# Kernel optimization log

Measured on AMD Instinct MI355X. Metric: run time of the kernel, lower is better.

The kernel has to match this reference:

```python
import jax, jax.numpy as jnp
import numpy as np

B, T, H = 64, 1024, 1024


def setup_inputs() -> dict:
    key = jax.random.key(0)
    ks = jax.random.split(key, 8)
    s = 1.0 / np.sqrt(H)
    return {
        "spatial_feats": jax.random.normal(ks[0], (B, T, H), dtype=jnp.float32),
        "hidden_state": jax.random.normal(ks[1], (B, H), dtype=jnp.float32),
        "W_enc": jax.random.uniform(ks[2], (H, H), jnp.float32, -s, s),
        "b_enc": jax.random.uniform(ks[3], (H,), jnp.float32, -s, s),
        "W_dec": jax.random.uniform(ks[4], (H, H), jnp.float32, -s, s),
        "b_dec": jax.random.uniform(ks[5], (H,), jnp.float32, -s, s),
        "w_score": jax.random.uniform(ks[6], (H,), jnp.float32, -s, s),
        "b_score": jax.random.uniform(ks[7], (), jnp.float32, -s, s),
    }


def reference(spatial_feats, hidden_state, W_enc, b_enc, W_dec, b_dec, w_score, b_score):
    # decoder_proj(hidden_state): [B, H] -> [B, 1, H]
    dec = (jnp.einsum("bh,oh->bo", hidden_state, W_dec) + b_dec)[:, None, :]
    # encoder_proj(spatial_feats): [B, T, H]
    enc = jnp.einsum("bth,oh->bto", spatial_feats, W_enc) + b_enc
    energy = jnp.tanh(enc + dec)                      # [B, T, H]
    scores = jnp.einsum("bth,h->bt", energy, w_score) + b_score  # [B, T]
    weights = jax.nn.softmax(scores, axis=1)          # [B, T]
    context = jnp.einsum("bth,bt->bh", spatial_feats, weights)   # [B, H]
    return (context, weights)
```

## Files before the change

kernel.cpp:

```cpp
#include <hip/hip_runtime.h>
#include <hip/hip_bf16.h>
#include <math.h>


typedef __attribute__((ext_vector_type(8))) short bf16x8;
typedef __attribute__((ext_vector_type(8))) unsigned short ushort8;
typedef __attribute__((ext_vector_type(4))) float f32x4;

__device__ __forceinline__ unsigned short f2bf(float f) {
  union { float f; unsigned int u; } v; v.f = f;
  unsigned int r = v.u + 0x7FFFu + ((v.u >> 16) & 1u);
  return (unsigned short)(r >> 16);
}

__device__ __forceinline__ float bf2f(unsigned short b) {
  union { unsigned int u; float f; } v; v.u = ((unsigned int)b) << 16;
  return v.f;
}

__device__ __forceinline__ float fast_tanh(float x) {
  float e = __expf(2.0f * x);
  return 1.0f - 2.0f / (e + 1.0f);
}

__device__ __forceinline__ void gld16(const void* g, void* l) {
  __builtin_amdgcn_global_load_lds(
      (const __attribute__((address_space(1))) void*)g,
      (__attribute__((address_space(3))) void*)l, 16, 0, 0);
}

__global__ __launch_bounds__(256) void prep_kernel(
    const float* __restrict__ spatial, const float* __restrict__ hidden,
    const float* __restrict__ W_enc, const float* __restrict__ b_enc,
    const float* __restrict__ W_dec, const float* __restrict__ b_dec,
    unsigned short* __restrict__ Wbf, unsigned short* __restrict__ Abf,
    float* __restrict__ dec, int nW, int nA) {
  __shared__ float hs[1024];
  const int bid = blockIdx.x, tid = threadIdx.x;
  if (bid < nW + nA) {
    const float* src = (bid < nW) ? W_enc : spatial;
    unsigned short* dst = (bid < nW) ? Wbf : Abf;
    size_t g4 = (size_t)(bid < nW ? bid : bid - nW) * 256 + tid;
    float4 v = ((const float4*)src)[g4];
    ushort4 o;
    o.x = f2bf(v.x); o.y = f2bf(v.y); o.z = f2bf(v.z); o.w = f2bf(v.w);
    *(ushort4*)(dst + g4 * 4) = o;
    return;
  }
  const int dbid = bid - nW - nA;
  const int b = dbid >> 3, o0 = (dbid & 7) * 128;
  const int wave = tid >> 6, lane = tid & 63;
  ((float4*)hs)[tid] = ((const float4*)(hidden + (size_t)b * 1024))[tid];
  __syncthreads();
  for (int it = 0; it < 32; it++) {
    int o = o0 + it * 4 + wave;
    const float4* w4 = (const float4*)(W_dec + (size_t)o * 1024);
    float4 acc; acc.x = acc.y = acc.z = acc.w = 0.f;
    #pragma unroll
    for (int j = 0; j < 4; j++) {
      int i = j * 64 + lane;
      float4 x = ((const float4*)hs)[i], y = w4[i];
      acc.x = fmaf(x.x, y.x, acc.x);
      acc.y = fmaf(x.y, y.y, acc.y);
      acc.z = fmaf(x.z, y.z, acc.z);
      acc.w = fmaf(x.w, y.w, acc.w);
    }
    float v = (acc.x + acc.y) + (acc.z + acc.w);
    #pragma unroll
    for (int off = 1; off < 64; off <<= 1) v += __shfl_xor(v, off);
    if (lane == 0) dec[b * 1024 + o] = v + b_dec[o] + b_enc[o];
  }
}

__global__ __launch_bounds__(256) void enc_score_bf16_kernel(
    const unsigned short* __restrict__ A,
    const unsigned short* __restrict__ W,
    const float* __restrict__ dec,
    const float* __restrict__ w_score,
    float* __restrict__ scores_p)
{
  __shared__ unsigned short As[2][128][32];
  __shared__ unsigned short Bs[2][128][32];

  const int bid = blockIdx.x;
  const int swz = (bid & 7) * 512 + (bid >> 3);
  const int n0 = (swz & 7) * 128;
  const int m0 = (swz >> 3) * 128;
  const int tid = threadIdx.x;
  const int lane = tid & 63, wave = tid >> 6;
  const int wm = (wave >> 1) * 64, wn = (wave & 1) * 64;
  const int quad = lane >> 4, colL = lane & 15;

  const int srow = wave * 32 + (lane >> 2);
  const int scol = (lane & 3) * 8;
  const unsigned short* ga = A + (size_t)(m0 + srow) * 1024 + scol;
  const unsigned short* gb = W + (size_t)(n0 + srow) * 1024 + scol;
  unsigned short* la = &As[0][0][0] + wave * 1024;
  unsigned short* lb = &Bs[0][0][0] + wave * 1024;

  f32x4 acc[4][4];
  #pragma unroll
  for (int mi = 0; mi < 4; mi++)
    #pragma unroll
    for (int ni = 0; ni < 4; ni++)
      acc[mi][ni] = (f32x4){0.f, 0.f, 0.f, 0.f};

  for (int k0 = 0; k0 < 1024; k0 += 64) {
    gld16(ga + k0,                  la);
    gld16(ga + k0 + 16 * 1024,      la + 512);
    gld16(ga + k0 + 32,             la + 4096);
    gld16(ga + k0 + 32 + 16 * 1024, la + 4608);
    gld16(gb + k0,                  lb);
    gld16(gb + k0 + 16 * 1024,      lb + 512);
    gld16(gb + k0 + 32,             lb + 4096);
    gld16(gb + k0 + 32 + 16 * 1024, lb + 4608);
    __syncthreads();
    #pragma unroll
    for (int h = 0; h < 2; h++) {
      bf16x8 af[4], bfr[4];
      #pragma unroll
      for (int i = 0; i < 4; i++) {
        af[i]  = *(const bf16x8*)(&As[h][wm + i * 16 + colL][quad * 8]);
        bfr[i] = *(const bf16x8*)(&Bs[h][wn + i * 16 + colL][quad * 8]);
      }
      #pragma unroll
      for (int mi = 0; mi < 4; mi++)
        #pragma unroll
        for (int ni = 0; ni < 4; ni++)
          acc[mi][ni] = __builtin_amdgcn_mfma_f32_16x16x32_bf16(
              af[mi], bfr[ni], acc[mi][ni], 0, 0, 0);
    }
    __syncthreads();
  }

  const int b = m0 >> 10;
  float decv[4], wsv[4];
  #pragma unroll
  for (int ni = 0; ni < 4; ni++) {
    int n = n0 + wn + ni * 16 + colL;
    decv[ni] = dec[b * 1024 + n];
    wsv[ni] = w_score[n];
  }
  const int slot = (swz & 7) * 2 + (wave & 1);
  #pragma unroll
  for (int mi = 0; mi < 4; mi++) {
    float rs[4] = {0.f, 0.f, 0.f, 0.f};
    #pragma unroll
    for (int ni = 0; ni < 4; ni++)
      #pragma unroll
      for (int r = 0; r < 4; r++)
        rs[r] += fast_tanh(acc[mi][ni][r] + decv[ni]) * wsv[ni];
    #pragma unroll
    for (int r = 0; r < 4; r++) {
      float v = rs[r];
      v += __shfl_xor(v, 1);
      v += __shfl_xor(v, 2);
      v += __shfl_xor(v, 4);
      v += __shfl_xor(v, 8);
      if (colL == 0)
        scores_p[slot * 65536 + m0 + wm + mi * 16 + quad * 4 + r] = v;
    }
  }
}

__global__ __launch_bounds__(256) void enc_score_f32_kernel(
    const float* __restrict__ A, const float* __restrict__ W,
    const float* __restrict__ dec, const float* __restrict__ w_score,
    float* __restrict__ scores_p) {
  __shared__ unsigned short As[128][32];
  __shared__ unsigned short Bs[128][32];
  const int bid = blockIdx.x;
  const int n0 = (bid & 7) * 128;
  const int m0 = (bid >> 3) * 128;
  const int tid = threadIdx.x;
  const int lane = tid & 63, wave = tid >> 6;
  const int wm = (wave >> 1) * 64, wn = (wave & 1) * 64;
  const int quad = lane >> 4, colL = lane & 15;
  const int srow = tid >> 3;
  const int scol = (tid & 7) * 4;
  f32x4 acc[4][4];
  #pragma unroll
  for (int mi = 0; mi < 4; mi++)
    #pragma unroll
    for (int ni = 0; ni < 4; ni++)
      acc[mi][ni] = (f32x4){0.f, 0.f, 0.f, 0.f};
  for (int k0 = 0; k0 < 1024; k0 += 32) {
    #pragma unroll
    for (int p = 0; p < 4; p++) {
      int r = p * 32 + srow;
      float4 va = *(const float4*)(A + (size_t)(m0 + r) * 1024 + (k0 + scol));
      float4 vb = *(const float4*)(W + (size_t)(n0 + r) * 1024 + (k0 + scol));
      ushort4 pa, pb;
      pa.x = f2bf(va.x); pa.y = f2bf(va.y); pa.z = f2bf(va.z); pa.w = f2bf(va.w);
      pb.x = f2bf(vb.x); pb.y = f2bf(vb.y); pb.z = f2bf(vb.z); pb.w = f2bf(vb.w);
      *(ushort4*)(&As[r][scol]) = pa;
      *(ushort4*)(&Bs[r][scol]) = pb;
    }
    __syncthreads();
    bf16x8 af[4], bfr[4];
    #pragma unroll
    for (int i = 0; i < 4; i++) {
      af[i]  = *(const bf16x8*)(&As[wm + i * 16 + colL][quad * 8]);
      bfr[i] = *(const bf16x8*)(&Bs[wn + i * 16 + colL][quad * 8]);
    }
    #pragma unroll
    for (int mi = 0; mi < 4; mi++)
      #pragma unroll
      for (int ni = 0; ni < 4; ni++)
        acc[mi][ni] = __builtin_amdgcn_mfma_f32_16x16x32_bf16(
            af[mi], bfr[ni], acc[mi][ni], 0, 0, 0);
    __syncthreads();
  }
  const int b = m0 >> 10;
  float decv[4], wsv[4];
  #pragma unroll
  for (int ni = 0; ni < 4; ni++) {
    int n = n0 + wn + ni * 16 + colL;
    decv[ni] = dec[b * 1024 + n];
    wsv[ni] = w_score[n];
  }
  const int slot = (bid & 7) * 2 + (wave & 1);
  #pragma unroll
  for (int mi = 0; mi < 4; mi++) {
    float rsv[4] = {0.f, 0.f, 0.f, 0.f};
    #pragma unroll
    for (int ni = 0; ni < 4; ni++)
      #pragma unroll
      for (int r = 0; r < 4; r++)
        rsv[r] += fast_tanh(acc[mi][ni][r] + decv[ni]) * wsv[ni];
    #pragma unroll
    for (int r = 0; r < 4; r++) {
      float v = rsv[r];
      v += __shfl_xor(v, 1);
      v += __shfl_xor(v, 2);
      v += __shfl_xor(v, 4);
      v += __shfl_xor(v, 8);
      if (colL == 0)
        scores_p[slot * 65536 + m0 + wm + mi * 16 + quad * 4 + r] = v;
    }
  }
}

__global__ void softmax_kernel(const float* __restrict__ scores_p,
                               float* __restrict__ weights,
                               float* __restrict__ context) {
  __shared__ float red[256];
  int b = blockIdx.x, tid = threadIdx.x;
  float4 z; z.x = z.y = z.z = z.w = 0.f;
  ((float4*)context)[blockIdx.x * 256 + tid] = z;
  float v[4];
  float mx = -1e30f;
  #pragma unroll
  for (int i = 0; i < 4; i++) {
    int m = b * 1024 + tid + i * 256;
    float s = 0.f;
    #pragma unroll
    for (int sl = 0; sl < 16; sl++) s += scores_p[sl * 65536 + m];
    v[i] = s;
    mx = fmaxf(mx, v[i]);
  }
  red[tid] = mx; __syncthreads();
  for (int off = 128; off > 0; off >>= 1) {
    if (tid < off) red[tid] = fmaxf(red[tid], red[tid + off]);
    __syncthreads();
  }
  mx = red[0]; __syncthreads();
  float sum = 0.f;
  #pragma unroll
  for (int i = 0; i < 4; i++) { v[i] = __expf(v[i] - mx); sum += v[i]; }
  red[tid] = sum; __syncthreads();
  for (int off = 128; off > 0; off >>= 1) {
    if (tid < off) red[tid] += red[tid + off];
    __syncthreads();
  }
  float inv = 1.0f / red[0];
  #pragma unroll
  for (int i = 0; i < 4; i++) weights[b * 1024 + tid + i * 256] = v[i] * inv;
}

__global__ void context_bf16_kernel(const unsigned short* __restrict__ Abf,
                                    const float* __restrict__ weights,
                                    float* __restrict__ context) {
  int b = blockIdx.x >> 3, tq = blockIdx.x & 7;
  int tid = threadIdx.x;
  __shared__ float wl[128];
  __shared__ float cs[128 * 8];
  if (tid < 128) wl[tid] = weights[b * 1024 + tq * 128 + tid];
  __syncthreads();
  const int hl = tid & 127, p = tid >> 7;
  const int h0 = hl * 8;
  const unsigned short* sp =
      Abf + ((size_t)(b * 1024 + tq * 128 + p)) * 1024 + h0;
  float acc[8];
  #pragma unroll
  for (int j = 0; j < 8; j++) acc[j] = 0.f;
  for (int t = 0; t < 128; t += 2) {
    float w = wl[t + p];
    ushort8 x = *(const ushort8*)(sp + (size_t)t * 1024);
    #pragma unroll
    for (int j = 0; j < 8; j++) acc[j] = fmaf(w, bf2f(x[j]), acc[j]);
  }
  if (p == 0) {
    #pragma unroll
    for (int j = 0; j < 8; j++) cs[hl * 8 + j] = acc[j];
  }
  __syncthreads();
  if (p == 1) {
    #pragma unroll
    for (int j = 0; j < 8; j++) cs[hl * 8 + j] += acc[j];
  }
  __syncthreads();
  if (p == 0) {
    #pragma unroll
    for (int j = 0; j < 8; j++)
      atomicAdd(&context[b * 1024 + h0 + j], cs[hl * 8 + j]);
  }
}

__global__ void context_f32_kernel(const float* __restrict__ spatial,
                                   const float* __restrict__ weights,
                                   float* __restrict__ context) {
  int b = blockIdx.x >> 3, tq = blockIdx.x & 7;
  int tid = threadIdx.x;
  __shared__ float wl[128];
  if (tid < 128) wl[tid] = weights[b * 1024 + tq * 128 + tid];
  __syncthreads();
  const float4* sp =
      (const float4*)(spatial + ((size_t)(b * 1024 + tq * 128)) * 1024);
  float4 acc; acc.x = acc.y = acc.z = acc.w = 0.f;
  #pragma unroll 4
  for (int t = 0; t < 128; t++) {
    float w = wl[t];
    float4 x = sp[(size_t)t * 256 + tid];
    acc.x = fmaf(w, x.x, acc.x);
    acc.y = fmaf(w, x.y, acc.y);
    acc.z = fmaf(w, x.z, acc.z);
    acc.w = fmaf(w, x.w, acc.w);
  }
  float* c = context + b * 1024 + tid * 4;
  atomicAdd(c + 0, acc.x);
  atomicAdd(c + 1, acc.y);
  atomicAdd(c + 2, acc.z);
  atomicAdd(c + 3, acc.w);
}

extern "C" void kernel_launch(void* const* d_in, const int* in_sizes, int n_in,
                              void* d_out, int out_size, void* d_ws, size_t ws_size,
                              hipStream_t stream) {
  const float* spatial  = (const float*)d_in[0];
  const float* hidden   = (const float*)d_in[1];
  const float* W_enc    = (const float*)d_in[2];
  const float* b_enc    = (const float*)d_in[3];
  const float* W_dec    = (const float*)d_in[4];
  const float* b_dec    = (const float*)d_in[5];
  const float* w_score  = (const float*)d_in[6];

  float* out      = (float*)d_out;
  float* context  = out;
  float* weights  = out + 65536;

  float* scores_p = (float*)d_ws;
  float* dec      = scores_p + 16 * 65536;
  unsigned short* Wbf = (unsigned short*)(dec + 65536);
  unsigned short* Abf = Wbf + 1024 * 1024;

  const size_t need =
      16ull * 65536 * 4 + 65536 * 4 + 2ull * 1024 * 1024 + 2ull * 65536 * 1024;

  if (ws_size >= need) {
    const int nW = 1024, nA = 65536;
    prep_kernel<<<nW + nA + 512, 256, 0, stream>>>(
        spatial, hidden, W_enc, b_enc, W_dec, b_dec, Wbf, Abf, dec, nW, nA);
    enc_score_bf16_kernel<<<4096, 256, 0, stream>>>(Abf, Wbf, dec, w_score,
                                                    scores_p);
    softmax_kernel<<<64, 256, 0, stream>>>(scores_p, weights, context);
    context_bf16_kernel<<<512, 256, 0, stream>>>(Abf, weights, context);
  } else {
    prep_kernel<<<512, 256, 0, stream>>>(
        spatial, hidden, W_enc, b_enc, W_dec, b_dec, nullptr, nullptr, dec,
        0, 0);
    enc_score_f32_kernel<<<4096, 256, 0, stream>>>(spatial, W_enc, dec,
                                                   w_score, scores_p);
    softmax_kernel<<<64, 256, 0, stream>>>(scores_p, weights, context);
    context_f32_kernel<<<512, 256, 0, stream>>>(spatial, weights, context);
  }
}
```

Before: 670.6 us.

## Triple-buffer GEMM K-loop with async LDS loads and coarsen bf16 conversion

The encoder GEMM now uses a three-stage ring buffer of 32-wide K tiles in LDS. It issues global-to-LDS loads two tiles ahead and waits with a partial vmcnt and one barrier per tile, replacing the old load-sync-compute-sync loop. MFMA sections are wrapped in s_setprio to favour compute waves. Separately, the bf16 conversion in the prep kernel runs with far fewer blocks, each looping over 32 float4 chunks, which cuts block launch overhead. The risks are higher LDS use, which may lower occupancy, and correctness depending on the hand-written vmcnt counting.

Result: faster. 654.4 us (-2.4%).

```diff
diff --git a/kernel.cpp b/kernel.cpp
--- a/kernel.cpp
+++ b/kernel.cpp
@@ -34,20 +34,25 @@
     const float* __restrict__ W_enc, const float* __restrict__ b_enc,
     const float* __restrict__ W_dec, const float* __restrict__ b_dec,
     unsigned short* __restrict__ Wbf, unsigned short* __restrict__ Abf,
-    float* __restrict__ dec, int nW, int nA) {
+    float* __restrict__ dec, int nCvt) {
   __shared__ float hs[1024];
   const int bid = blockIdx.x, tid = threadIdx.x;
-  if (bid < nW + nA) {
-    const float* src = (bid < nW) ? W_enc : spatial;
-    unsigned short* dst = (bid < nW) ? Wbf : Abf;
-    size_t g4 = (size_t)(bid < nW ? bid : bid - nW) * 256 + tid;
-    float4 v = ((const float4*)src)[g4];
-    ushort4 o;
-    o.x = f2bf(v.x); o.y = f2bf(v.y); o.z = f2bf(v.z); o.w = f2bf(v.w);
-    *(ushort4*)(dst + g4 * 4) = o;
+  if (bid < nCvt) {
+    const bool isW = bid < 32;
+    const float* src = isW ? W_enc : spatial;
+    unsigned short* dst = isW ? Wbf : Abf;
+    const size_t base = (size_t)(isW ? bid : bid - 32) * 8192 + tid;
+    #pragma unroll 4
+    for (int i = 0; i < 32; i++) {
+      size_t g4 = base + (size_t)i * 256;
+      float4 v = ((const float4*)src)[g4];
+      ushort4 o;
+      o.x = f2bf(v.x); o.y = f2bf(v.y); o.z = f2bf(v.z); o.w = f2bf(v.w);
+      *(ushort4*)(dst + g4 * 4) = o;
+    }
     return;
   }
-  const int dbid = bid - nW - nA;
+  const int dbid = bid - nCvt;
   const int b = dbid >> 3, o0 = (dbid & 7) * 128;
   const int wave = tid >> 6, lane = tid & 63;
   ((float4*)hs)[tid] = ((const float4*)(hidden + (size_t)b * 1024))[tid];
@@ -79,8 +84,8 @@
     const float* __restrict__ w_score,
     float* __restrict__ scores_p)
 {
-  __shared__ unsigned short As[2][128][32];
-  __shared__ unsigned short Bs[2][128][32];
+  __shared__ unsigned short As[3][128][32];
+  __shared__ unsigned short Bs[3][128][32];
 
   const int bid = blockIdx.x;
   const int swz = (bid & 7) * 512 + (bid >> 3);
@@ -105,33 +110,51 @@
     for (int ni = 0; ni < 4; ni++)
       acc[mi][ni] = (f32x4){0.f, 0.f, 0.f, 0.f};
 
-  for (int k0 = 0; k0 < 1024; k0 += 64) {
-    gld16(ga + k0,                  la);
-    gld16(ga + k0 + 16 * 1024,      la + 512);
-    gld16(ga + k0 + 32,             la + 4096);
-    gld16(ga + k0 + 32 + 16 * 1024, la + 4608);
-    gld16(gb + k0,                  lb);
-    gld16(gb + k0 + 16 * 1024,      lb + 512);
-    gld16(gb + k0 + 32,             lb + 4096);
-    gld16(gb + k0 + 32 + 16 * 1024, lb + 4608);
-    __syncthreads();
-    #pragma unroll
-    for (int h = 0; h < 2; h++) {
-      bf16x8 af[4], bfr[4];
+  auto stage_tile = [&](int t, int b) {
+    const unsigned short* ga_ = ga + t * 32;
+    const unsigned short* gb_ = gb + t * 32;
+    unsigned short* la_ = la + b * 4096;
+    unsigned short* lb_ = lb + b * 4096;
+    gld16(ga_,             la_);
+    gld16(ga_ + 16 * 1024, la_ + 512);
+    gld16(gb_,             lb_);
+    gld16(gb_ + 16 * 1024, lb_ + 512);
+  };
+
+  auto compute_tile = [&](int b) {
+    bf16x8 af[4], bfr[4];
+    #pragma unroll
+    for (int i = 0; i < 4; i++) {
+      af[i]  = *(const bf16x8*)(&As[b][wm + i * 16 + colL][quad * 8]);
+      bfr[i] = *(const bf16x8*)(&Bs[b][wn + i * 16 + colL][quad * 8]);
+    }
+    __builtin_amdgcn_s_setprio(1);
+    #pragma unroll
+    for (int mi = 0; mi < 4; mi++)
       #pragma unroll
-      for (int i = 0; i < 4; i++) {
-        af[i]  = *(const bf16x8*)(&As[h][wm + i * 16 + colL][quad * 8]);
-        bfr[i] = *(const bf16x8*)(&Bs[h][wn + i * 16 + colL][quad * 8]);
-      }
-      #pragma unroll
-      for (int mi = 0; mi < 4; mi++)
-        #pragma unroll
-        for (int ni = 0; ni < 4; ni++)
-          acc[mi][ni] = __builtin_amdgcn_mfma_f32_16x16x32_bf16(
-              af[mi], bfr[ni], acc[mi][ni], 0, 0, 0);
-    }
-    __syncthreads();
-  }
+      for (int ni = 0; ni < 4; ni++)
+        acc[mi][ni] = __builtin_amdgcn_mfma_f32_16x16x32_bf16(
+            af[mi], bfr[ni], acc[mi][ni], 0, 0, 0);
+    __builtin_amdgcn_s_setprio(0);
+  };
+
+  stage_tile(0, 0);
+  stage_tile(1, 1);
+
+  int buf = 0;
+  for (int t = 0; t < 31; t++) {
+    asm volatile("s_waitcnt vmcnt(4)" ::: "memory");
+    __builtin_amdgcn_s_barrier();
+    if (t < 30) {
+      int b2 = buf + 2; if (b2 >= 3) b2 -= 3;
+      stage_tile(t + 2, b2);
+    }
+    compute_tile(buf);
+    buf = (buf == 2) ? 0 : buf + 1;
+  }
+  asm volatile("s_waitcnt vmcnt(0)" ::: "memory");
+  __builtin_amdgcn_s_barrier();
+  compute_tile(buf);
 
   const int b = m0 >> 10;
   float decv[4], wsv[4];
@@ -368,9 +391,9 @@
       16ull * 65536 * 4 + 65536 * 4 + 2ull * 1024 * 1024 + 2ull * 65536 * 1024;
 
   if (ws_size >= need) {
-    const int nW = 1024, nA = 65536;
-    prep_kernel<<<nW + nA + 512, 256, 0, stream>>>(
-        spatial, hidden, W_enc, b_enc, W_dec, b_dec, Wbf, Abf, dec, nW, nA);
+    const int nCvt = 32 + 2048;
+    prep_kernel<<<nCvt + 512, 256, 0, stream>>>(
+        spatial, hidden, W_enc, b_enc, W_dec, b_dec, Wbf, Abf, dec, nCvt);
     enc_score_bf16_kernel<<<4096, 256, 0, stream>>>(Abf, Wbf, dec, w_score,
                                                     scores_p);
     softmax_kernel<<<64, 256, 0, stream>>>(scores_p, weights, context);
@@ -378,7 +401,7 @@
   } else {
     prep_kernel<<<512, 256, 0, stream>>>(
         spatial, hidden, W_enc, b_enc, W_dec, b_dec, nullptr, nullptr, dec,
-        0, 0);
+        0);
     enc_score_f32_kernel<<<4096, 256, 0, stream>>>(spatial, W_enc, dec,
                                                    w_score, scores_p);
     softmax_kernel<<<64, 256, 0, stream>>>(scores_p, weights, context);
```
